# Kernel tuning notes

Hardware: AMD Instinct MI355X
Metric: run time of the kernel (lower is better)

Reference implementation:

```python
import jax, jax.numpy as jnp
import numpy as np

GROUPS = 2048   # number of FPS centroids S
K = 24          # ball-query neighbors
RADIUS = 0.2    # ball radius (xyz in unit cube)


def setup_inputs() -> dict:
    key = jax.random.key(0)
    k1, k2 = jax.random.split(key)
    xyz = jax.random.uniform(k1, (8, 8192, 3), dtype=jnp.float32)
    points = jax.random.normal(k2, (8, 8192, 128), dtype=jnp.float32)
    return {"xyz": xyz, "points": points}


def _fps(xyz, npoint):
    # iterative farthest point sampling; deterministic start at index 0
    B, N, _ = xyz.shape

    def step(carry, _):
        distance, farthest = carry                       # [B,N], [B]
        centroid = jnp.take_along_axis(xyz, farthest[:, None, None], axis=1)  # [B,1,3]
        d = jnp.sum((xyz - centroid) ** 2, axis=-1)      # [B,N]
        distance = jnp.minimum(distance, d)
        nxt = jnp.argmax(distance, axis=-1).astype(jnp.int32)
        return (distance, nxt), farthest

    init = (jnp.full((B, N), 1e10, jnp.float32), jnp.zeros((B,), jnp.int32))
    _, idxs = jax.lax.scan(step, init, None, length=npoint)  # [npoint,B]
    return jnp.transpose(idxs)                               # [B,npoint]


def _index_points(points, idx):
    # points [B,N,C], idx [B,...] -> [B,...,C]
    B = idx.shape[0]
    flat = idx.reshape(B, -1)
    out = jnp.take_along_axis(points, flat[..., None], axis=1)
    return out.reshape(*idx.shape, points.shape[-1])


def _square_distance(src, dst):
    # src [B,N,C], dst [B,M,C] -> [B,N,M]
    return (jnp.sum(src ** 2, -1)[..., None]
            + jnp.sum(dst ** 2, -1)[:, None, :]
            - 2.0 * jnp.einsum('bnc,bmc->bnm', src, dst))


def _query_ball(radius, nsample, xyz, new_xyz):
    B, N, _ = xyz.shape
    sqr = _square_distance(new_xyz, xyz)                 # [B,S,N]
    base = jnp.arange(N, dtype=jnp.int32)
    idx = jnp.where(sqr > radius * radius, jnp.int32(N), base)  # out-of-ball -> N
    idx = jnp.sort(idx, axis=-1)[..., :nsample]          # [B,S,k]
    first = idx[..., :1]
    return jnp.where(idx == N, first, idx)


def reference(xyz, points):
    B, N, _ = xyz.shape
    fps_idx = _fps(xyz, GROUPS)                          # [B,S]
    new_xyz = _index_points(xyz, fps_idx)                # [B,S,3]
    anchor_feat = _index_points(points, fps_idx)         # [B,S,D]
    idx = _query_ball(RADIUS, K, xyz, new_xyz)           # [B,S,k]
    grouped_xyz = _index_points(xyz, idx)                # [B,S,k,3]
    grouped_points = _index_points(points, idx)          # [B,S,k,D]
    grouped = jnp.concatenate([grouped_points, grouped_xyz], axis=-1)  # use_xyz=True
    anchor = jnp.broadcast_to(anchor_feat[:, :, None, :],
                              (B, GROUPS, K, points.shape[-1]))
    new_points = jnp.concatenate([grouped, anchor], axis=-1)  # [B,S,k,2D+3]
    return new_xyz, new_points
```

## Files before the change

kernel.cpp:

```cpp
#include <hip/hip_runtime.h>
#include <stdint.h>


#define NBATCH 8
#define NPTS   8192
#define NCH    128
#define NGROUP 2048
#define NK     24
#define ROWLEN (2 * NCH + 3)

#define FPS_T   512
#define PPT     16
#define GBLOCKS 248
#define GSLOTS  62
#define GITERS  34

typedef float v2f __attribute__((ext_vector_type(2)));

struct __attribute__((packed, aligned(4))) f4s { float x, y, z, w; };

__device__ __forceinline__ float sq3_nofma(float dx, float dy, float dz) {
#pragma clang fp contract(off)
  return dx * dx + dy * dy + dz * dz;
}

__device__ __forceinline__ float dot3_fma(float ax, float ay, float az,
                                          float bx, float by, float bz) {
  float acc = __fmul_rn(ax, bx);
  acc = __fmaf_rn(ay, by, acc);
  acc = __fmaf_rn(az, bz, acc);
  return acc;
}

__device__ __forceinline__ float ballquery_sqr(float srcSq, float dstSq, float dot) {
#pragma clang fp contract(off)
  return (srcSq + dstSq) - 2.0f * dot;
}

template <int CTRL>
__device__ __forceinline__ float maxdpp(float v) {
  int s = __builtin_amdgcn_update_dpp(__builtin_bit_cast(int, v),
                                      __builtin_bit_cast(int, v),
                                      CTRL, 0xF, 0xF, false);
  return fmaxf(v, __builtin_bit_cast(float, s));
}

__device__ __forceinline__ float readlane_f(float v, int lane) {
  return __builtin_bit_cast(float,
      __builtin_amdgcn_readlane(__builtin_bit_cast(int, v), lane));
}

__global__ __launch_bounds__(FPS_T) void fused_kernel(const float* __restrict__ xyz,
                                                      const float* __restrict__ points,
                                                      int* __restrict__ fps_idx,
                                                      float* __restrict__ out) {
  const int t = threadIdx.x;

  __shared__ float s_xyz[NPTS * 3];
  union pair_t { struct { float v; int i; }; unsigned long long u; };
  __shared__ __align__(16) pair_t s_p[2][8];
  __shared__ int s_aidx[2];
  __shared__ int s_idx2[2][NK];

  if (blockIdx.x < NBATCH) {
    const int b = blockIdx.x;
    const int lane = t & 63;
    const int w = t >> 6;
    const float* xb = xyz + (size_t)b * NPTS * 3;

    {
      const float4* src4 = (const float4*)xb;
      float4* dst4 = (float4*)s_xyz;
      for (int i = t; i < (NPTS * 3) / 4; i += FPS_T) dst4[i] = src4[i];
    }

    const int base = t * PPT;
    v2f px[8], py[8], pz[8], d2[8];
#pragma unroll
    for (int j = 0; j < 8; ++j) {
      const int n0 = base + 2 * j;
      px[j].x = xb[n0 * 3 + 0]; py[j].x = xb[n0 * 3 + 1]; pz[j].x = xb[n0 * 3 + 2];
      px[j].y = xb[n0 * 3 + 3]; py[j].y = xb[n0 * 3 + 4]; pz[j].y = xb[n0 * 3 + 5];
      d2[j].x = 1e10f; d2[j].y = 1e10f;
    }

    float cx = xb[0], cy = xb[1], cz = xb[2];
    if (t == 0)
      __hip_atomic_store(&fps_idx[b * NGROUP + 0], 0,
                         __ATOMIC_RELAXED, __HIP_MEMORY_SCOPE_AGENT);

    for (int s = 1; s < NGROUP; ++s) {
      const int p = s & 1;

      float lv = -1.0f;
#pragma unroll
      for (int j = 0; j < 8; ++j) {
        v2f dx, dy, dz, dd, nd;
        {
#pragma clang fp contract(off)
          dx = px[j] - cx;
          dy = py[j] - cy;
          dz = pz[j] - cz;
          dd = dx * dx + dy * dy + dz * dz;
        }
        nd.x = fminf(d2[j].x, dd.x);
        nd.y = fminf(d2[j].y, dd.y);
        d2[j] = nd;
        lv = fmaxf(fmaxf(nd.x, nd.y), lv);
      }
      int kk = 0;
#pragma unroll
      for (int j = 7; j >= 0; --j) {
        if (d2[j].y == lv) kk = 2 * j + 1;
        if (d2[j].x == lv) kk = 2 * j;
      }
      const int li = base + kk;

      float v = lv;
      v = maxdpp<0x111>(v);
      v = maxdpp<0x112>(v);
      v = maxdpp<0x114>(v);
      v = maxdpp<0x118>(v);
      v = maxdpp<0x142>(v);
      v = maxdpp<0x143>(v);
      const float wmax = readlane_f(v, 63);
      const unsigned long long m = __ballot(lv == wmax);
      const int wl = (int)__builtin_ctzll(m);
      const int wli = __builtin_amdgcn_readlane(li, wl);
      if (lane == 0) {
        s_p[p][w].u = ((unsigned long long)(unsigned)wli << 32) |
                      (unsigned long long)__builtin_bit_cast(unsigned, wmax);
      }
      __syncthreads();

      const float4* q = (const float4*)&s_p[p][0];
      const float4 q0 = q[0], q1 = q[1], q2 = q[2], q3 = q[3];
      float bv = q0.x;
      float biF = q0.y;
      {
        const float vv[7] = { q0.z, q1.x, q1.z, q2.x, q2.z, q3.x, q3.z };
        const float ii[7] = { q0.w, q1.y, q1.w, q2.y, q2.w, q3.y, q3.w };
#pragma unroll
        for (int k = 0; k < 7; ++k) {
          const bool gt = vv[k] > bv;
          bv  = gt ? vv[k] : bv;
          biF = gt ? ii[k] : biF;
        }
      }
      const int bi = __builtin_bit_cast(int, biF);

      if (t == 0)
        __hip_atomic_store(&fps_idx[b * NGROUP + s], bi,
                           __ATOMIC_RELAXED, __HIP_MEMORY_SCOPE_AGENT);

      const int b3 = bi * 3;
      cx = s_xyz[b3 + 0];
      cy = s_xyz[b3 + 1];
      cz = s_xyz[b3 + 2];
    }
    return;
  }

  const int gs = blockIdx.x - NBATCH;
  const int b = gs & 7;
  const int sb = gs >> 3;
  const int h = t >> 8;
  const int htid = t & 255;
  const float* xb = xyz + (size_t)b * NPTS * 3;
  const float* pb = points + (size_t)b * NPTS * NCH;
  const float R2 = (float)(0.2 * 0.2);

  for (int i = 0; i < GITERS; ++i) {
    const int g = i * GSLOTS + sb * 2 + h;
    const bool act = g < NGROUP;
    const int gb = (b << 11) | (g & 2047);

    if (htid == 0 && act) {
      int v;
      while ((v = __hip_atomic_load(&fps_idx[gb], __ATOMIC_RELAXED,
                                    __HIP_MEMORY_SCOPE_AGENT)) == -1)
        __builtin_amdgcn_s_sleep(8);
      s_aidx[h] = v;
    }
    __syncthreads();

    int a_idx = 0;
    float cx = 0.f, cy = 0.f, cz = 0.f, srcSq = 0.f;
    if (act) {
      a_idx = s_aidx[h];
      cx = xb[a_idx * 3 + 0];
      cy = xb[a_idx * 3 + 1];
      cz = xb[a_idx * 3 + 2];
      srcSq = sq3_nofma(cx, cy, cz);

      if (htid < 64) {
        int cnt = 0;
        int first = 0;
        const unsigned long long below = ((unsigned long long)1 << htid) - 1ull;
        for (int chunk = 0; chunk < NPTS / 128; ++chunk) {
          const int n0 = (chunk << 7) + (htid << 1);
          const float* p = xb + (size_t)n0 * 3;
          const float2 A = *(const float2*)(p + 0);
          const float2 Bv = *(const float2*)(p + 2);
          const float2 C = *(const float2*)(p + 4);
          const float x0 = A.x, y0 = A.y, z0 = Bv.x;
          const float x1 = Bv.y, y1 = C.x, z1 = C.y;

          const float sqr0 = ballquery_sqr(srcSq, sq3_nofma(x0, y0, z0),
                                           dot3_fma(cx, cy, cz, x0, y0, z0));
          const float sqr1 = ballquery_sqr(srcSq, sq3_nofma(x1, y1, z1),
                                           dot3_fma(cx, cy, cz, x1, y1, z1));
          const bool ok0 = !(sqr0 > R2);
          const bool ok1 = !(sqr1 > R2);
          const unsigned long long m0 = __ballot(ok0);
          const unsigned long long m1 = __ballot(ok1);
          if (cnt == 0 && (m0 | m1)) {
            const int f0 = m0 ? (int)__builtin_ctzll(m0) : 64;
            const int f1 = m1 ? (int)__builtin_ctzll(m1) : 64;
            first = (f0 <= f1) ? ((chunk << 7) + 2 * f0) : ((chunk << 7) + 2 * f1 + 1);
          }
          const int p0 = cnt + (int)__popcll(m0 & below) + (int)__popcll(m1 & below);
          const int p1 = p0 + (ok0 ? 1 : 0);
          if (ok0 && p0 < NK) s_idx2[h][p0] = n0;
          if (ok1 && p1 < NK) s_idx2[h][p1] = n0 + 1;
          cnt += (int)__popcll(m0) + (int)__popcll(m1);
          if (cnt >= NK) break;
        }
        if (htid >= cnt && htid < NK) s_idx2[h][htid] = first;
      }
    }
    __syncthreads();

    if (act) {
      if (htid == 0) {
        float* onx = out + (size_t)gb * 3;
        onx[0] = cx; onx[1] = cy; onx[2] = cz;
      }

      float* op = out + (size_t)NBATCH * NGROUP * 3 + (size_t)gb * (NK * ROWLEN);
      const float* anchor = pb + (size_t)a_idx * NCH;

#pragma unroll
      for (int it = 0; it < 3; ++it) {
        const int vidx = htid + (it << 8);
        const int k = vidx >> 5;
        const int c4 = vidx & 31;
        const int si = s_idx2[h][k];
        const f4s val = *(const f4s*)(pb + (size_t)si * NCH + (c4 << 2));
        *(f4s*)(op + k * ROWLEN + (c4 << 2)) = val;
      }
#pragma unroll
      for (int it = 0; it < 3; ++it) {
        const int vidx = htid + (it << 8);
        const int k = vidx >> 5;
        const int c4 = vidx & 31;
        const f4s val = *(const f4s*)(anchor + (c4 << 2));
        *(f4s*)(op + k * ROWLEN + (NCH + 3) + (c4 << 2)) = val;
      }
      if (htid < NK * 3) {
        const int k = htid / 3;
        const int r = htid - k * 3;
        const int si = s_idx2[h][k];
        op[k * ROWLEN + NCH + r] = xb[si * 3 + r];
      }
    }
    __syncthreads();
  }
}

extern "C" void kernel_launch(void* const* d_in, const int* in_sizes, int n_in,
                              void* d_out, int out_size, void* d_ws, size_t ws_size,
                              hipStream_t stream) {
  const float* xyz = (const float*)d_in[0];
  const float* points = (const float*)d_in[1];
  float* out = (float*)d_out;
  int* fps_idx = (int*)d_ws;

  hipMemsetAsync(d_ws, 0xFF, (size_t)NBATCH * NGROUP * sizeof(int), stream);
  fused_kernel<<<dim3(NBATCH + GBLOCKS), dim3(FPS_T), 0, stream>>>(xyz, points, fps_idx, out);
}
```

Measured before the change: 2.034 ms.

## Split farthest point sampling per batch across four cooperating blocks via global slots

Each batch's FPS loop is now spread over four workgroups, each owning a quarter of the points. Every step they exchange their local argmax through packed value/step/index words in global memory and spin until all four have published. This cuts per-thread distance work and register use per step, but adds a cross-CU global-memory handshake on each of the 2047 serial iterations. It also takes CUs away from the grouping blocks, whose count drops to keep the grid at 256.

```diff
diff --git a/kernel.cpp b/kernel.cpp
--- a/kernel.cpp
+++ b/kernel.cpp
@@ -9,13 +9,16 @@
 #define NK     24
 #define ROWLEN (2 * NCH + 3)
 
-#define FPS_T   512
-#define PPT     16
-#define GBLOCKS 248
-#define GSLOTS  62
-#define GITERS  34
+#define FPS_T    512
+#define FPS_KS   4
+#define FPS_BLKS (NBATCH * FPS_KS)
+#define BLK_PTS  (NPTS / FPS_KS)
+#define GBLOCKS  (256 - FPS_BLKS)
+#define GSLOTS   ((GBLOCKS / NBATCH) * 2)
+#define GITERS   ((NGROUP + GSLOTS - 1) / GSLOTS)
 
 typedef float v2f __attribute__((ext_vector_type(2)));
+typedef unsigned long long u64;
 
 struct __attribute__((packed, aligned(4))) f4s { float x, y, z, w; };
 
@@ -53,20 +56,23 @@
 __global__ __launch_bounds__(FPS_T) void fused_kernel(const float* __restrict__ xyz,
                                                       const float* __restrict__ points,
                                                       int* __restrict__ fps_idx,
+                                                      u64* __restrict__ slots,
                                                       float* __restrict__ out) {
   const int t = threadIdx.x;
 
   __shared__ float s_xyz[NPTS * 3];
-  union pair_t { struct { float v; int i; }; unsigned long long u; };
+  union pair_t { struct { float v; int i; }; u64 u; };
   __shared__ __align__(16) pair_t s_p[2][8];
   __shared__ int s_aidx[2];
   __shared__ int s_idx2[2][NK];
 
-  if (blockIdx.x < NBATCH) {
-    const int b = blockIdx.x;
+  if (blockIdx.x < FPS_BLKS) {
+    const int b = blockIdx.x & 7;
+    const int k = blockIdx.x >> 3;
     const int lane = t & 63;
     const int w = t >> 6;
     const float* xb = xyz + (size_t)b * NPTS * 3;
+    u64* bslots = slots + (size_t)b * 2 * FPS_KS;
 
     {
       const float4* src4 = (const float4*)xb;
@@ -74,10 +80,10 @@
       for (int i = t; i < (NPTS * 3) / 4; i += FPS_T) dst4[i] = src4[i];
     }
 
-    const int base = t * PPT;
-    v2f px[8], py[8], pz[8], d2[8];
-#pragma unroll
-    for (int j = 0; j < 8; ++j) {
+    const int base = k * BLK_PTS + (t << 2);
+    v2f px[2], py[2], pz[2], d2[2];
+#pragma unroll
+    for (int j = 0; j < 2; ++j) {
       const int n0 = base + 2 * j;
       px[j].x = xb[n0 * 3 + 0]; py[j].x = xb[n0 * 3 + 1]; pz[j].x = xb[n0 * 3 + 2];
       px[j].y = xb[n0 * 3 + 3]; py[j].y = xb[n0 * 3 + 4]; pz[j].y = xb[n0 * 3 + 5];
@@ -85,7 +91,7 @@
     }
 
     float cx = xb[0], cy = xb[1], cz = xb[2];
-    if (t == 0)
+    if (k == 0 && t == 0)
       __hip_atomic_store(&fps_idx[b * NGROUP + 0], 0,
                          __ATOMIC_RELAXED, __HIP_MEMORY_SCOPE_AGENT);
 
@@ -94,7 +100,7 @@
 
       float lv = -1.0f;
 #pragma unroll
-      for (int j = 0; j < 8; ++j) {
+      for (int j = 0; j < 2; ++j) {
         v2f dx, dy, dz, dd, nd;
         {
 #pragma clang fp contract(off)
@@ -109,11 +115,10 @@
         lv = fmaxf(fmaxf(nd.x, nd.y), lv);
       }
       int kk = 0;
-#pragma unroll
-      for (int j = 7; j >= 0; --j) {
-        if (d2[j].y == lv) kk = 2 * j + 1;
-        if (d2[j].x == lv) kk = 2 * j;
-      }
+      if (d2[1].y == lv) kk = 3;
+      if (d2[1].x == lv) kk = 2;
+      if (d2[0].y == lv) kk = 1;
+      if (d2[0].x == lv) kk = 0;
       const int li = base + kk;
 
       float v = lv;
@@ -124,12 +129,12 @@
       v = maxdpp<0x142>(v);
       v = maxdpp<0x143>(v);
       const float wmax = readlane_f(v, 63);
-      const unsigned long long m = __ballot(lv == wmax);
+      const u64 m = __ballot(lv == wmax);
       const int wl = (int)__builtin_ctzll(m);
       const int wli = __builtin_amdgcn_readlane(li, wl);
       if (lane == 0) {
-        s_p[p][w].u = ((unsigned long long)(unsigned)wli << 32) |
-                      (unsigned long long)__builtin_bit_cast(unsigned, wmax);
+        s_p[p][w].u = ((u64)(unsigned)wli << 32) |
+                      (u64)__builtin_bit_cast(unsigned, wmax);
       }
       __syncthreads();
 
@@ -141,19 +146,51 @@
         const float vv[7] = { q0.z, q1.x, q1.z, q2.x, q2.z, q3.x, q3.z };
         const float ii[7] = { q0.w, q1.y, q1.w, q2.y, q2.w, q3.y, q3.w };
 #pragma unroll
-        for (int k = 0; k < 7; ++k) {
-          const bool gt = vv[k] > bv;
-          bv  = gt ? vv[k] : bv;
-          biF = gt ? ii[k] : biF;
-        }
-      }
-      const int bi = __builtin_bit_cast(int, biF);
-
-      if (t == 0)
-        __hip_atomic_store(&fps_idx[b * NGROUP + s], bi,
+        for (int e = 0; e < 7; ++e) {
+          const bool gt = vv[e] > bv;
+          bv  = gt ? vv[e] : bv;
+          biF = gt ? ii[e] : biF;
+        }
+      }
+      const int blk_i = __builtin_bit_cast(int, biF);
+
+      if (t == 0) {
+        const u64 pk = ((u64)__builtin_bit_cast(unsigned, bv) << 32) |
+                       ((u64)(unsigned)s << 13) | (u64)(unsigned)blk_i;
+        __hip_atomic_store(&bslots[p * FPS_KS + k], pk,
                            __ATOMIC_RELAXED, __HIP_MEMORY_SCOPE_AGENT);
-
-      const int b3 = bi * 3;
+      }
+
+      float gv; int gi;
+      {
+        u64 sl[FPS_KS];
+#pragma unroll
+        for (int k2 = 0; k2 < FPS_KS; ++k2) {
+          u64 vv2;
+          while ((unsigned)(((vv2 = __hip_atomic_load(&bslots[p * FPS_KS + k2],
+                                                      __ATOMIC_RELAXED,
+                                                      __HIP_MEMORY_SCOPE_AGENT))
+                             >> 13) & 0x7FF) != (unsigned)s)
+            __builtin_amdgcn_s_sleep(1);
+          sl[k2] = vv2;
+        }
+        gv = __builtin_bit_cast(float, (unsigned)(sl[0] >> 32));
+        gi = (int)(sl[0] & 0x1FFF);
+#pragma unroll
+        for (int k2 = 1; k2 < FPS_KS; ++k2) {
+          const float v2 = __builtin_bit_cast(float, (unsigned)(sl[k2] >> 32));
+          const int i2 = (int)(sl[k2] & 0x1FFF);
+          const bool gt = v2 > gv;
+          gv = gt ? v2 : gv;
+          gi = gt ? i2 : gi;
+        }
+      }
+
+      if (k == 0 && t == 0)
+        __hip_atomic_store(&fps_idx[b * NGROUP + s], gi,
+                           __ATOMIC_RELAXED, __HIP_MEMORY_SCOPE_AGENT);
+
+      const int b3 = gi * 3;
       cx = s_xyz[b3 + 0];
       cy = s_xyz[b3 + 1];
       cz = s_xyz[b3 + 2];
@@ -161,7 +198,7 @@
     return;
   }
 
-  const int gs = blockIdx.x - NBATCH;
+  const int gs = blockIdx.x - FPS_BLKS;
   const int b = gs & 7;
   const int sb = gs >> 3;
   const int h = t >> 8;
@@ -196,7 +233,7 @@
       if (htid < 64) {
         int cnt = 0;
         int first = 0;
-        const unsigned long long below = ((unsigned long long)1 << htid) - 1ull;
+        const u64 below = ((u64)1 << htid) - 1ull;
         for (int chunk = 0; chunk < NPTS / 128; ++chunk) {
           const int n0 = (chunk << 7) + (htid << 1);
           const float* p = xb + (size_t)n0 * 3;
@@ -212,8 +249,8 @@
                                            dot3_fma(cx, cy, cz, x1, y1, z1));
           const bool ok0 = !(sqr0 > R2);
           const bool ok1 = !(sqr1 > R2);
-          const unsigned long long m0 = __ballot(ok0);
-          const unsigned long long m1 = __ballot(ok1);
+          const u64 m0 = __ballot(ok0);
+          const u64 m1 = __ballot(ok1);
           if (cnt == 0 && (m0 | m1)) {
             const int f0 = m0 ? (int)__builtin_ctzll(m0) : 64;
             const int f1 = m1 ? (int)__builtin_ctzll(m1) : 64;
@@ -243,25 +280,25 @@
 #pragma unroll
       for (int it = 0; it < 3; ++it) {
         const int vidx = htid + (it << 8);
-        const int k = vidx >> 5;
+        const int kx = vidx >> 5;
         const int c4 = vidx & 31;
-        const int si = s_idx2[h][k];
+        const int si = s_idx2[h][kx];
         const f4s val = *(const f4s*)(pb + (size_t)si * NCH + (c4 << 2));
-        *(f4s*)(op + k * ROWLEN + (c4 << 2)) = val;
+        *(f4s*)(op + kx * ROWLEN + (c4 << 2)) = val;
       }
 #pragma unroll
       for (int it = 0; it < 3; ++it) {
         const int vidx = htid + (it << 8);
-        const int k = vidx >> 5;
+        const int kx = vidx >> 5;
         const int c4 = vidx & 31;
         const f4s val = *(const f4s*)(anchor + (c4 << 2));
-        *(f4s*)(op + k * ROWLEN + (NCH + 3) + (c4 << 2)) = val;
+        *(f4s*)(op + kx * ROWLEN + (NCH + 3) + (c4 << 2)) = val;
       }
       if (htid < NK * 3) {
-        const int k = htid / 3;
-        const int r = htid - k * 3;
-        const int si = s_idx2[h][k];
-        op[k * ROWLEN + NCH + r] = xb[si * 3 + r];
+        const int kx = htid / 3;
+        const int r = htid - kx * 3;
+        const int si = s_idx2[h][kx];
+        op[kx * ROWLEN + NCH + r] = xb[si * 3 + r];
       }
     }
     __syncthreads();
@@ -275,7 +312,11 @@
   const float* points = (const float*)d_in[1];
   float* out = (float*)d_out;
   int* fps_idx = (int*)d_ws;
-
-  hipMemsetAsync(d_ws, 0xFF, (size_t)NBATCH * NGROUP * sizeof(int), stream);
-  fused_kernel<<<dim3(NBATCH + GBLOCKS), dim3(FPS_T), 0, stream>>>(xyz, points, fps_idx, out);
-}
+  u64* slots = (u64*)((char*)d_ws + (size_t)NBATCH * NGROUP * sizeof(int));
+
+  hipMemsetAsync(d_ws, 0xFF,
+                 (size_t)NBATCH * NGROUP * sizeof(int) +
+                 (size_t)NBATCH * 2 * FPS_KS * sizeof(u64), stream);
+  fused_kernel<<<dim3(FPS_BLKS + GBLOCKS), dim3(FPS_T), 0, stream>>>(
+      xyz, points, fps_idx, slots, out);
+}
```

Result: slower. 3.871 ms (+90.3%).
